# Kernel tuning notes

Hardware: AMD Instinct MI355X
Metric: run time of the kernel (lower is better)

## Reference

```python
import jax, jax.numpy as jnp
import numpy as np

B, N, F_IN, F_OUT = 8, 2048, 128, 128


def setup_inputs() -> dict:
    key = jax.random.key(0)
    k1, k2, k3, k4 = jax.random.split(key, 4)
    h = jax.random.normal(k1, (B, N, F_IN), dtype=jnp.float32)
    adj = (jax.random.uniform(k2, (B, N, N)) > 0.5).astype(jnp.float32)
    adj = jnp.maximum(adj, jnp.eye(N, dtype=jnp.float32)[None])
    # torch nn.Linear weights: W is [out_features, in_features], a is [1, 2*out_features]
    W = jax.random.normal(k3, (F_OUT, F_IN), dtype=jnp.float32) * 0.05
    a = jax.random.normal(k4, (1, 2 * F_OUT), dtype=jnp.float32) * 0.05
    return {"h": h, "adj": adj, "W": W, "a": a}


def reference(h, adj, W, a):
    # Wh = W(h): [B, N, F_OUT]
    Wh = jnp.einsum("bnf,of->bno", h, W)
    # attn_fc(concat(Wh_i, Wh_j)) == (Wh_i @ a1) + (Wh_j @ a2): exact split of the
    # linear layer, avoiding the O(B*N*N*2F) concat intermediate.
    a1 = a[0, :F_OUT]
    a2 = a[0, F_OUT:]
    e_i = Wh @ a1  # [B, N]  score contribution of destination node i
    e_j = Wh @ a2  # [B, N]  score contribution of source node j
    e = e_i[:, :, None] + e_j[:, None, :]  # [B, N, N]
    e = e + (1.0 - adj) * (-1e9)
    alpha = jax.nn.softmax(e, axis=-1)  # [B, N, N]
    # weighted aggregation: h_out[b,i] = sum_j alpha[b,i,j] * Wh[b,j]
    h_out = jnp.einsum("bij,bjo->bio", alpha, Wh)
    return h_out
```

## Files before the change

kernel.cpp:

```cpp
#include <hip/hip_runtime.h>
#include <stdint.h>

#define AS1 __attribute__((address_space(1)))
#define AS3 __attribute__((address_space(3)))

typedef __bf16 bf16x8 __attribute__((ext_vector_type(8)));
typedef float f32x4 __attribute__((ext_vector_type(4)));

constexpr int NB = 8;
constexpr int N  = 2048;
constexpr int F  = 128;

__device__ __forceinline__ unsigned short bf16r(float f) {
    unsigned u = __float_as_uint(f);
    return (unsigned short)((u + 0x7FFFu + ((u >> 16) & 1u)) >> 16);
}
__device__ __forceinline__ float bf2f(unsigned short s) {
    return __uint_as_float(((unsigned)s) << 16);
}


__global__ __launch_bounds__(256) void k1_wh(const float* __restrict__ h,
                                             const float* __restrict__ W,
                                             const float* __restrict__ a,
                                             unsigned short* __restrict__ Wb2,
                                             unsigned short* __restrict__ p16) {
    __shared__ float epart[2][64];

    const int tid  = threadIdx.x;
    const int lane = tid & 63, wid = tid >> 6;
    const int quad = lane >> 4, l15 = lane & 15;
    const int wm = wid >> 1, wn = wid & 1;
    const int m0 = blockIdx.x * 64;
    const int batch = m0 >> 11;
    const int nbase = m0 & 2047;

    f32x4 acc[2][4] = {};

#pragma unroll
    for (int kk = 0; kk < 4; ++kk) {
        const int k = kk * 32 + quad * 8;
        bf16x8 afr[2], bfr[4];
#pragma unroll
        for (int rt = 0; rt < 2; ++rt) {
            const float* src = h + (size_t)(m0 + wm * 32 + rt * 16 + l15) * F + k;
            float4 x0 = *(const float4*)src;
            float4 x1 = *(const float4*)(src + 4);
            afr[rt][0] = (__bf16)x0.x; afr[rt][1] = (__bf16)x0.y;
            afr[rt][2] = (__bf16)x0.z; afr[rt][3] = (__bf16)x0.w;
            afr[rt][4] = (__bf16)x1.x; afr[rt][5] = (__bf16)x1.y;
            afr[rt][6] = (__bf16)x1.z; afr[rt][7] = (__bf16)x1.w;
        }
#pragma unroll
        for (int ct = 0; ct < 4; ++ct) {
            const int o = wn * 64 + ct * 16 + l15;
            const float* src = W + (size_t)o * F + k;
            float4 x0 = *(const float4*)src;
            float4 x1 = *(const float4*)(src + 4);
            bfr[ct][0] = (__bf16)x0.x; bfr[ct][1] = (__bf16)x0.y;
            bfr[ct][2] = (__bf16)x0.z; bfr[ct][3] = (__bf16)x0.w;
            bfr[ct][4] = (__bf16)x1.x; bfr[ct][5] = (__bf16)x1.y;
            bfr[ct][6] = (__bf16)x1.z; bfr[ct][7] = (__bf16)x1.w;
        }
#pragma unroll
        for (int rt = 0; rt < 2; ++rt)
#pragma unroll
            for (int ct = 0; ct < 4; ++ct)
                acc[rt][ct] = __builtin_amdgcn_mfma_f32_16x16x32_bf16(
                    afr[rt], bfr[ct], acc[rt][ct], 0, 0, 0);
    }

    float a2v[4];
#pragma unroll
    for (int ct = 0; ct < 4; ++ct) a2v[ct] = a[F + wn * 64 + ct * 16 + l15];

    float ep[2][4];
#pragma unroll
    for (int rt = 0; rt < 2; ++rt)
#pragma unroll
        for (int g = 0; g < 4; ++g) {
            float s = 0.f;
#pragma unroll
            for (int ct = 0; ct < 4; ++ct) s += acc[rt][ct][g] * a2v[ct];
            ep[rt][g] = s;
        }
#pragma unroll
    for (int m = 1; m < 16; m <<= 1)
#pragma unroll
        for (int rt = 0; rt < 2; ++rt)
#pragma unroll
            for (int g = 0; g < 4; ++g)
                ep[rt][g] += __shfl_xor(ep[rt][g], m);

    if (l15 == 0)
#pragma unroll
        for (int rt = 0; rt < 2; ++rt)
#pragma unroll
            for (int g = 0; g < 4; ++g)
                epart[wn][wm * 32 + rt * 16 + quad * 4 + g] = ep[rt][g];
    __syncthreads();

#pragma unroll
    for (int rt = 0; rt < 2; ++rt)
#pragma unroll
        for (int ct = 0; ct < 4; ++ct) {
            const int o  = wn * 64 + ct * 16 + l15;
            const int r0 = wm * 32 + rt * 16 + quad * 4;
            const int n0 = nbase + r0;
            ushort4 v;
#pragma unroll
            for (int g = 0; g < 4; ++g) {
                const float e  = epart[0][r0 + g] + epart[1][r0 + g];
                const float pf = bf2f(bf16r(expf(e)));
                (&v.x)[g] = bf16r(pf * acc[rt][ct][g]);
            }
            size_t off = (size_t)batch * N * F + (size_t)(n0 >> 3) * 1024 + o * 8 + (n0 & 7);
            *(ushort4*)&Wb2[off] = v;
        }

    if (tid < 64) {
        const float e = epart[0][tid] + epart[1][tid];
        p16[batch * N + nbase + tid] = bf16r(expf(e));
    }
}

__global__ __launch_bounds__(256, 2) void k3_fused(const float* __restrict__ adj,
                                                   const unsigned short* __restrict__ Wb2,
                                                   const unsigned short* __restrict__ p16,
                                                   float* __restrict__ out) {
    const int tid  = threadIdx.x;
    const int lane = tid & 63, wid = tid >> 6;
    const int quad = lane >> 4, l15 = lane & 15;
    const int wm = wid >> 1, wn = wid & 1;
    const int b  = blockIdx.x & 7;
    const int it = blockIdx.x >> 3;
    const int i0 = it * 32;
    const int rowA = i0 + wm * 16 + l15;

    const float* aP = adj + (size_t)b * N * N + (size_t)rowA * N + quad * 8;
    const char*  bP = (const char*)Wb2 + (size_t)b * (N * F * 2)
                    + quad * 2048 + wn * 1024 + l15 * 16;
    const char*  pP = (const char*)p16 + (size_t)b * N * 2 + quad * 16;

    f32x4 acc[4] = {};
    f32x4 dacc = {0.f, 0.f, 0.f, 0.f};

    f32x4  a0n = *(const f32x4*)(aP);
    f32x4  a1n = *(const f32x4*)(aP + 4);
    bf16x8 bn0 = *(const bf16x8*)(bP + 0 * 256);
    bf16x8 bn1 = *(const bf16x8*)(bP + 1 * 256);
    bf16x8 bn2 = *(const bf16x8*)(bP + 2 * 256);
    bf16x8 bn3 = *(const bf16x8*)(bP + 3 * 256);
    bf16x8 pn  = *(const bf16x8*)(pP);

#pragma unroll 2
    for (int c = 0; c < 64; ++c) {
        f32x4  a0 = a0n, a1 = a1n;
        bf16x8 b0 = bn0, b1 = bn1, b2 = bn2, b3 = bn3, pv = pn;
        if (c + 1 < 64) {
            const float* aN = aP + (size_t)(c + 1) * 32;
            const char*  bN = bP + (size_t)(c + 1) * 8192;
            a0n = *(const f32x4*)(aN);
            a1n = *(const f32x4*)(aN + 4);
            bn0 = *(const bf16x8*)(bN + 0 * 256);
            bn1 = *(const bf16x8*)(bN + 1 * 256);
            bn2 = *(const bf16x8*)(bN + 2 * 256);
            bn3 = *(const bf16x8*)(bN + 3 * 256);
            pn  = *(const bf16x8*)(pP + (size_t)(c + 1) * 64);
        }
        bf16x8 af;
        af[0] = (__bf16)a0[0]; af[1] = (__bf16)a0[1];
        af[2] = (__bf16)a0[2]; af[3] = (__bf16)a0[3];
        af[4] = (__bf16)a1[0]; af[5] = (__bf16)a1[1];
        af[6] = (__bf16)a1[2]; af[7] = (__bf16)a1[3];

        acc[0] = __builtin_amdgcn_mfma_f32_16x16x32_bf16(af, b0, acc[0], 0, 0, 0);
        acc[1] = __builtin_amdgcn_mfma_f32_16x16x32_bf16(af, b1, acc[1], 0, 0, 0);
        acc[2] = __builtin_amdgcn_mfma_f32_16x16x32_bf16(af, b2, acc[2], 0, 0, 0);
        acc[3] = __builtin_amdgcn_mfma_f32_16x16x32_bf16(af, b3, acc[3], 0, 0, 0);
        dacc   = __builtin_amdgcn_mfma_f32_16x16x32_bf16(af, pv, dacc,   0, 0, 0);
    }

#pragma unroll
    for (int g = 0; g < 4; ++g) {
        const float inv = 1.0f / dacc[g];
        float* orow = out + ((size_t)b * N + i0 + wm * 16 + quad * 4 + g) * F
                    + wn * 64 + l15;
        orow[0]  = acc[0][g] * inv;
        orow[16] = acc[1][g] * inv;
        orow[32] = acc[2][g] * inv;
        orow[48] = acc[3][g] * inv;
    }
}

extern "C" void kernel_launch(void* const* d_in, const int* in_sizes, int n_in,
                              void* d_out, int out_size, void* d_ws, size_t ws_size,
                              hipStream_t stream) {
    const float* h   = (const float*)d_in[0];
    const float* adj = (const float*)d_in[1];
    const float* W   = (const float*)d_in[2];
    const float* a   = (const float*)d_in[3];
    float* out = (float*)d_out;

    unsigned short* Wb2 = (unsigned short*)d_ws;
    unsigned short* p16 = (unsigned short*)((char*)d_ws + (4u << 20));

    k1_wh<<<NB * N / 64, 256, 0, stream>>>(h, W, a, Wb2, p16);
    k3_fused<<<NB * 64, 256, 0, stream>>>(adj, Wb2, p16, out);
}
```

Before: 228.6 us.

## Pack adjacency into bitmask in first kernel and rebuild bf16 operands from bits

The first kernel gains extra blocks that ballot-compress the fp32 adjacency matrix into a 1-bit-per-entry mask in workspace. The aggregation kernel then reads the compact mask and expands bits directly into bf16 1.0/0.0 MFMA A-fragments, with a new warp tiling: each wave covers both 16-row tiles and 32 output columns. The full fp32 adjacency is still read once, but the bandwidth-heavy fused kernel now streams far less data. The cost is an extra mask write and read, plus bit-expansion ALU work per MFMA.

```diff
diff --git a/kernel.cpp b/kernel.cpp
--- a/kernel.cpp
+++ b/kernel.cpp
@@ -6,6 +6,7 @@
 
 typedef __bf16 bf16x8 __attribute__((ext_vector_type(8)));
 typedef float f32x4 __attribute__((ext_vector_type(4)));
+typedef unsigned int u32x4 __attribute__((ext_vector_type(4)));
 
 constexpr int NB = 8;
 constexpr int N  = 2048;
@@ -20,15 +21,40 @@
 }
 
 
-__global__ __launch_bounds__(256) void k1_wh(const float* __restrict__ h,
-                                             const float* __restrict__ W,
-                                             const float* __restrict__ a,
-                                             unsigned short* __restrict__ Wb2,
-                                             unsigned short* __restrict__ p16) {
-    __shared__ float epart[2][64];
-
+__global__ __launch_bounds__(256) void k01_wh(const float* __restrict__ h,
+                                              const float* __restrict__ adj,
+                                              const float* __restrict__ W,
+                                              const float* __restrict__ a,
+                                              unsigned short* __restrict__ Wb2,
+                                              unsigned short* __restrict__ p16,
+                                              unsigned char* __restrict__ maskG) {
     const int tid  = threadIdx.x;
     const int lane = tid & 63, wid = tid >> 6;
+
+    if (blockIdx.x >= 256) {
+        const int cid = blockIdx.x - 256;
+#pragma unroll
+        for (int rr = 0; rr < 2; ++rr) {
+            const int row = cid * 8 + wid * 2 + rr;
+            const float2* src = (const float2*)(adj + (size_t)row * 2048) + lane;
+            u32x4* dst = (u32x4*)(maskG + (size_t)row * 256);
+#pragma unroll 4
+            for (int t = 0; t < 16; ++t) {
+                float2 v = src[t * 64];
+                unsigned long long m0 = __ballot(v.x > 0.5f);
+                unsigned long long m1 = __ballot(v.y > 0.5f);
+                if (lane == 0) {
+                    u32x4 w = { (unsigned)m0, (unsigned)(m0 >> 32),
+                                (unsigned)m1, (unsigned)(m1 >> 32) };
+                    dst[t] = w;
+                }
+            }
+        }
+        return;
+    }
+
+    __shared__ float epart[2][64];
+
     const int quad = lane >> 4, l15 = lane & 15;
     const int wm = wid >> 1, wn = wid & 1;
     const int m0 = blockIdx.x * 64;
@@ -124,73 +150,74 @@
     }
 }
 
-__global__ __launch_bounds__(256, 2) void k3_fused(const float* __restrict__ adj,
+__global__ __launch_bounds__(256, 2) void k3_fused(const unsigned char* __restrict__ maskG,
                                                    const unsigned short* __restrict__ Wb2,
                                                    const unsigned short* __restrict__ p16,
                                                    float* __restrict__ out) {
     const int tid  = threadIdx.x;
     const int lane = tid & 63, wid = tid >> 6;
     const int quad = lane >> 4, l15 = lane & 15;
-    const int wm = wid >> 1, wn = wid & 1;
     const int b  = blockIdx.x & 7;
     const int it = blockIdx.x >> 3;
     const int i0 = it * 32;
-    const int rowA = i0 + wm * 16 + l15;
-
-    const float* aP = adj + (size_t)b * N * N + (size_t)rowA * N + quad * 8;
-    const char*  bP = (const char*)Wb2 + (size_t)b * (N * F * 2)
-                    + quad * 2048 + wn * 1024 + l15 * 16;
-    const char*  pP = (const char*)p16 + (size_t)b * N * 2 + quad * 16;
-
-    f32x4 acc[4] = {};
-    f32x4 dacc = {0.f, 0.f, 0.f, 0.f};
-
-    f32x4  a0n = *(const f32x4*)(aP);
-    f32x4  a1n = *(const f32x4*)(aP + 4);
-    bf16x8 bn0 = *(const bf16x8*)(bP + 0 * 256);
-    bf16x8 bn1 = *(const bf16x8*)(bP + 1 * 256);
-    bf16x8 bn2 = *(const bf16x8*)(bP + 2 * 256);
-    bf16x8 bn3 = *(const bf16x8*)(bP + 3 * 256);
-    bf16x8 pn  = *(const bf16x8*)(pP);
+
+    const u32x4* mrow0 = (const u32x4*)(maskG + (size_t)(b * 2048 + i0 + l15) * 256);
+    const u32x4* mrow1 = (const u32x4*)(maskG + (size_t)(b * 2048 + i0 + 16 + l15) * 256);
+    const char* wb = (const char*)Wb2 + (size_t)b * (N * F * 2)
+                   + quad * 2048 + (wid * 32 + l15) * 16;
+    const char* pp = (const char*)p16 + (size_t)b * N * 2 + quad * 16;
+
+    f32x4 acc[2][2] = {};
+    f32x4 dacc[2] = {};
 
 #pragma unroll 2
-    for (int c = 0; c < 64; ++c) {
-        f32x4  a0 = a0n, a1 = a1n;
-        bf16x8 b0 = bn0, b1 = bn1, b2 = bn2, b3 = bn3, pv = pn;
-        if (c + 1 < 64) {
-            const float* aN = aP + (size_t)(c + 1) * 32;
-            const char*  bN = bP + (size_t)(c + 1) * 8192;
-            a0n = *(const f32x4*)(aN);
-            a1n = *(const f32x4*)(aN + 4);
-            bn0 = *(const bf16x8*)(bN + 0 * 256);
-            bn1 = *(const bf16x8*)(bN + 1 * 256);
-            bn2 = *(const bf16x8*)(bN + 2 * 256);
-            bn3 = *(const bf16x8*)(bN + 3 * 256);
-            pn  = *(const bf16x8*)(pP + (size_t)(c + 1) * 64);
-        }
-        bf16x8 af;
-        af[0] = (__bf16)a0[0]; af[1] = (__bf16)a0[1];
-        af[2] = (__bf16)a0[2]; af[3] = (__bf16)a0[3];
-        af[4] = (__bf16)a1[0]; af[5] = (__bf16)a1[1];
-        af[6] = (__bf16)a1[2]; af[7] = (__bf16)a1[3];
-
-        acc[0] = __builtin_amdgcn_mfma_f32_16x16x32_bf16(af, b0, acc[0], 0, 0, 0);
-        acc[1] = __builtin_amdgcn_mfma_f32_16x16x32_bf16(af, b1, acc[1], 0, 0, 0);
-        acc[2] = __builtin_amdgcn_mfma_f32_16x16x32_bf16(af, b2, acc[2], 0, 0, 0);
-        acc[3] = __builtin_amdgcn_mfma_f32_16x16x32_bf16(af, b3, acc[3], 0, 0, 0);
-        dacc   = __builtin_amdgcn_mfma_f32_16x16x32_bf16(af, pv, dacc,   0, 0, 0);
-    }
-
-#pragma unroll
-    for (int g = 0; g < 4; ++g) {
-        const float inv = 1.0f / dacc[g];
-        float* orow = out + ((size_t)b * N + i0 + wm * 16 + quad * 4 + g) * F
-                    + wn * 64 + l15;
-        orow[0]  = acc[0][g] * inv;
-        orow[16] = acc[1][g] * inv;
-        orow[32] = acc[2][g] * inv;
-        orow[48] = acc[3][g] * inv;
-    }
+    for (int t = 0; t < 16; ++t) {
+        const u32x4 q0 = mrow0[t];
+        const u32x4 q1 = mrow1[t];
+#pragma unroll
+        for (int s = 0; s < 4; ++s) {
+            const int j0 = t * 128 + s * 32;
+            const char* bc = wb + (size_t)j0 * 256;
+            bf16x8 bf0 = *(const bf16x8*)(bc);
+            bf16x8 bf1 = *(const bf16x8*)(bc + 256);
+            bf16x8 pv  = *(const bf16x8*)(pp + j0 * 2);
+
+            const unsigned uE0 = (s >> 1) ? q0.y : q0.x;
+            const unsigned uO0 = (s >> 1) ? q0.w : q0.z;
+            const unsigned uE1 = (s >> 1) ? q1.y : q1.x;
+            const unsigned uO1 = (s >> 1) ? q1.w : q1.z;
+            const int base = (s & 1) * 16 + quad * 4;
+            u32x4 aw0, aw1;
+#pragma unroll
+            for (int i = 0; i < 4; ++i) {
+                const int bi = base + i;
+                aw0[i] = (((uE0 >> bi) & 1u) ? 0x00003F80u : 0u)
+                       | (((uO0 >> bi) & 1u) ? 0x3F800000u : 0u);
+                aw1[i] = (((uE1 >> bi) & 1u) ? 0x00003F80u : 0u)
+                       | (((uO1 >> bi) & 1u) ? 0x3F800000u : 0u);
+            }
+            bf16x8 af0 = __builtin_bit_cast(bf16x8, aw0);
+            bf16x8 af1 = __builtin_bit_cast(bf16x8, aw1);
+
+            acc[0][0] = __builtin_amdgcn_mfma_f32_16x16x32_bf16(af0, bf0, acc[0][0], 0, 0, 0);
+            acc[0][1] = __builtin_amdgcn_mfma_f32_16x16x32_bf16(af0, bf1, acc[0][1], 0, 0, 0);
+            acc[1][0] = __builtin_amdgcn_mfma_f32_16x16x32_bf16(af1, bf0, acc[1][0], 0, 0, 0);
+            acc[1][1] = __builtin_amdgcn_mfma_f32_16x16x32_bf16(af1, bf1, acc[1][1], 0, 0, 0);
+            dacc[0]   = __builtin_amdgcn_mfma_f32_16x16x32_bf16(af0, pv,  dacc[0],  0, 0, 0);
+            dacc[1]   = __builtin_amdgcn_mfma_f32_16x16x32_bf16(af1, pv,  dacc[1],  0, 0, 0);
+        }
+    }
+
+#pragma unroll
+    for (int rt = 0; rt < 2; ++rt)
+#pragma unroll
+        for (int g = 0; g < 4; ++g) {
+            const float inv = 1.0f / dacc[rt][g];
+            float* orow = out + ((size_t)b * N + i0 + rt * 16 + quad * 4 + g) * F
+                        + wid * 32 + l15;
+            orow[0]  = acc[rt][0][g] * inv;
+            orow[16] = acc[rt][1][g] * inv;
+        }
 }
 
 extern "C" void kernel_launch(void* const* d_in, const int* in_sizes, int n_in,
@@ -202,9 +229,10 @@
     const float* a   = (const float*)d_in[3];
     float* out = (float*)d_out;
 
-    unsigned short* Wb2 = (unsigned short*)d_ws;
-    unsigned short* p16 = (unsigned short*)((char*)d_ws + (4u << 20));
-
-    k1_wh<<<NB * N / 64, 256, 0, stream>>>(h, W, a, Wb2, p16);
-    k3_fused<<<NB * 64, 256, 0, stream>>>(adj, Wb2, p16, out);
-}
+    unsigned short* Wb2   = (unsigned short*)d_ws;
+    unsigned short* p16   = (unsigned short*)((char*)d_ws + (4u << 20));
+    unsigned char*  maskG = (unsigned char*)((char*)d_ws + (8u << 20));
+
+    k01_wh<<<256 + 2048, 256, 0, stream>>>(h, adj, W, a, Wb2, p16, maskG);
+    k3_fused<<<NB * 64, 256, 0, stream>>>(maskG, Wb2, p16, out);
+}
```

Result: slower. 240.6 us (+5.2%).
